# Kernel tuning notes

Hardware: AMD Instinct MI355X
Metric: run time of the kernel (lower is better)

## Reference

```python
import jax, jax.numpy as jnp
import numpy as np
from jax import lax

E = 5      # NUM_EXPERTS
K = 3      # top-k
DIN = 32 * 10 * 10  # 3200
DH = 128
NCLS = 10


def setup_inputs() -> dict:
    key = jax.random.key(0)
    ks = jax.random.split(key, 16)
    s = 0.02
    return {
        "x": jax.random.normal(ks[0], (8192, 1, 28, 28), dtype=jnp.float32),
        "conv1_w": jax.random.normal(ks[1], (16, 1, 5, 5), dtype=jnp.float32) * s,
        "conv1_b": jnp.zeros((16,), jnp.float32),
        "conv2_w": jax.random.normal(ks[2], (32, 16, 3, 3), dtype=jnp.float32) * s,
        "conv2_b": jnp.zeros((32,), jnp.float32),
        "Wg": jax.random.normal(ks[3], (DIN, E), dtype=jnp.float32) * s,
        "bg": jnp.zeros((E,), jnp.float32),
        "Wglu": jax.random.normal(ks[4], (DIN, E), dtype=jnp.float32) * s,
        "bglu": jnp.zeros((E,), jnp.float32),
        "W1e": jax.random.normal(ks[5], (E, DIN, DH), dtype=jnp.float32) * s,
        "b1e": jnp.zeros((E, DH), jnp.float32),
        "W2e": jax.random.normal(ks[6], (E, DH, DH), dtype=jnp.float32) * s,
        "b2e": jnp.zeros((E, DH), jnp.float32),
        "Ws": jax.random.normal(ks[7], (DH, NCLS), dtype=jnp.float32) * s,
        "bs": jnp.zeros((NCLS,), jnp.float32),
    }


def _conv(x, w, b):
    y = lax.conv_general_dilated(x, w, (1, 1), 'VALID',
                                 dimension_numbers=('NCHW', 'OIHW', 'NCHW'))
    return y + b[None, :, None, None]


def _maxpool2(x):
    return lax.reduce_window(x, -jnp.inf, lax.max, (1, 1, 2, 2), (1, 1, 2, 2), 'VALID')


def reference(x, conv1_w, conv1_b, conv2_w, conv2_b, Wg, bg, Wglu, bglu,
              W1e, b1e, W2e, b2e, Ws, bs):
    # conv feature extractor: [B,1,28,28] -> [B,3200]
    h = jax.nn.relu(_conv(x, conv1_w, conv1_b))          # [B,16,24,24]
    h = _maxpool2(h)                                     # [B,16,12,12]
    h = jax.nn.relu(_conv(h, conv2_w, conv2_b))          # [B,32,10,10]
    feat = h.reshape(h.shape[0], -1)                     # [B,3200]

    # GLU-gated router: logits * sigmoid(glu)
    h_act = feat @ Wg + bg                               # [B,E]
    h_glu_act = jax.nn.sigmoid(feat @ Wglu + bglu)       # [B,E]
    gate_logits = h_act * h_glu_act                      # [B,E]

    # top-K routing with softmax over selected logits
    top_v, top_i = lax.top_k(gate_logits, K)             # [B,K]
    top_w = jax.nn.softmax(top_v, axis=-1)               # [B,K]
    onehot = jax.nn.one_hot(top_i, E, dtype=feat.dtype)  # [B,K,E]
    weights = jnp.einsum('bk,bke->be', top_w, onehot)    # [B,E]

    # experts (dense compute of all E=5 experts, masked combine)
    e1 = jnp.tanh(jnp.einsum('bd,edh->beh', feat, W1e) + b1e[None])  # [B,E,128]
    e2 = jnp.tanh(jnp.einsum('beh,ehg->beg', e1, W2e) + b2e[None])   # [B,E,128]
    moe_out = jnp.einsum('beg,be->bg', e2, weights)      # [B,128]

    logits = moe_out @ Ws + bs                           # [B,10]
    return jax.nn.softmax(logits, axis=1)
```

## Files before the change

### kernel.cpp

```cpp
#include <hip/hip_runtime.h>
#include <stdint.h>

typedef unsigned short u16;
typedef __attribute__((ext_vector_type(8))) short bf16x8;
typedef __attribute__((ext_vector_type(4))) float f32x4;

#define MFMA16(a, b, c) __builtin_amdgcn_mfma_f32_16x16x32_bf16((a), (b), (c), 0, 0, 0)
#define GLD16(gp, lp) __builtin_amdgcn_global_load_lds( \
    (__attribute__((address_space(1))) void*)(gp), \
    (__attribute__((address_space(3))) void*)(lp), 16, 0, 0)

__device__ __forceinline__ u16 f2b(float f) {
  uint32_t u = __float_as_uint(f);
  u += 0x7FFFu + ((u >> 16) & 1u);
  return (u16)(u >> 16);
}
__device__ __forceinline__ float tanhfast(float x) {
  float e = __expf(2.f * x);
  return (e - 1.f) / (e + 1.f);
}


__global__ __launch_bounds__(256) void prep_misc_kernel(
    const float* __restrict__ c2w, const float* __restrict__ Wg,
    const float* __restrict__ Wglu, const float* __restrict__ W2e,
    u16* __restrict__ W2colF, u16* __restrict__ WcatT, u16* __restrict__ W2T) {
  int i = blockIdx.x * 256 + threadIdx.x;
  if (i < 5120) {
    int j = i & 7, l = (i >> 3) & 63, nt = (i >> 9) & 1, s = i >> 10;
    int k = s * 32 + ((l >> 4) & 3) * 8 + j;
    int n = (l & 15) + nt * 16;
    float v = 0.f;
    if (k < 144) {
      int kykx = k >> 4, ci = k & 15;
      int ky = kykx / 3, kx = kykx - ky * 3;
      v = c2w[((n * 16 + ci) * 3 + ky) * 3 + kx];
    }
    W2colF[i] = f2b(v);
  } else if (i < 56320) {
    int o = i - 5120;
    int s = o >> 9, rest = o & 511;
    int l = rest >> 3, j = rest & 7;
    int r = l & 15, c = (l >> 4) * 8 + j;
    int dref = c * 100 + s;
    float v = 0.f;
    if (r < 5) v = Wg[dref * 5 + r];
    else if (r < 10) v = Wglu[dref * 5 + (r - 5)];
    WcatT[o] = f2b(v);
  } else if (i < 138240) {
    int o = i - 56320;
    int e = o >> 14, rem = o & 16383;
    int g = rem >> 7, h = rem & 127;
    W2T[o] = f2b(W2e[(e * 128 + h) * 128 + g]);
  }
}

__global__ __launch_bounds__(256) void prep_w1t_kernel(
    const float* __restrict__ W1e, u16* __restrict__ W1T) {
  __shared__ u16 ts[64][128];
  int t = threadIdx.x;
  int e = blockIdx.x / 50, pt = blockIdx.x % 50;
  {
    int r64 = t >> 2;
    int ph = r64 >> 5, c = r64 & 31;
    int d = c * 100 + pt * 2 + ph;
    const float* src = W1e + ((size_t)e * 3200 + d) * 128 + (t & 3) * 32;
    u16* drow = &ts[r64][(t & 3) * 32];
#pragma unroll
    for (int u = 0; u < 8; u++) {
      float4 v = *(const float4*)(src + u * 4);
      drow[u * 4 + 0] = f2b(v.x); drow[u * 4 + 1] = f2b(v.y);
      drow[u * 4 + 2] = f2b(v.z); drow[u * 4 + 3] = f2b(v.w);
    }
  }
  __syncthreads();
#pragma unroll
  for (int k = 0; k < 4; k++) {
    int u = t + k * 256;
    int ph = u >> 9, nb = (u >> 6) & 7, l = u & 63;
    int lm = l & 15, lqf = l >> 4;
    u16 tmp[8];
#pragma unroll
    for (int j = 0; j < 8; j++)
      tmp[j] = ts[ph * 32 + lqf * 8 + j][nb * 16 + lm];
    *(uint4*)(W1T + (((size_t)((e * 100 + pt * 2 + ph) * 8 + nb)) << 9) + l * 8) =
        *(const uint4*)tmp;
  }
}

__global__ __launch_bounds__(256) void conv1_kernel(
    const float* __restrict__ x, const float* __restrict__ w1,
    const float* __restrict__ b1, u16* __restrict__ h1) {
  __shared__ __align__(16) u16 cp[7232];
  int t = threadIdx.x, b = blockIdx.x, w = t >> 6, l = t & 63;

  if (t < 84) {
    int r = (t * 171) >> 9;
    int o = t - r * 3;
    const float4* src = (const float4*)(x + (size_t)b * 784 + r * 28 + o * 8);
    float4 qa = src[0], qb = src[1], qc = src[2];
    float4 qd = {0.f, 0.f, 0.f, 0.f};
    if (o < 2) qd = src[3];
    uint32_t d0 = (uint32_t)f2b(qa.x) | ((uint32_t)f2b(qa.y) << 16);
    uint32_t d1 = (uint32_t)f2b(qa.z) | ((uint32_t)f2b(qa.w) << 16);
    uint32_t d2 = (uint32_t)f2b(qb.x) | ((uint32_t)f2b(qb.y) << 16);
    uint32_t d3 = (uint32_t)f2b(qb.z) | ((uint32_t)f2b(qb.w) << 16);
    uint32_t d4 = (uint32_t)f2b(qc.x) | ((uint32_t)f2b(qc.y) << 16);
    uint32_t d5 = (uint32_t)f2b(qc.z) | ((uint32_t)f2b(qc.w) << 16);
    uint32_t d6 = (uint32_t)f2b(qd.x) | ((uint32_t)f2b(qd.y) << 16);
    uint32_t d7 = (uint32_t)f2b(qd.z) | ((uint32_t)f2b(qd.w) << 16);
#define SH(hi, lo) (((lo) >> 16) | ((hi) << 16))
    int base = r * 32 + o * 8;
    *(uint4*)&cp[base + 0 * 904] = uint4{d0, d1, d2, d3};
    *(uint4*)&cp[base + 1 * 904] = uint4{SH(d1, d0), SH(d2, d1), SH(d3, d2), SH(d4, d3)};
    *(uint4*)&cp[base + 2 * 904] = uint4{d1, d2, d3, d4};
    *(uint4*)&cp[base + 3 * 904] = uint4{SH(d2, d1), SH(d3, d2), SH(d4, d3), SH(d5, d4)};
    *(uint4*)&cp[base + 4 * 904] = uint4{d2, d3, d4, d5};
    *(uint4*)&cp[base + 5 * 904] = uint4{SH(d3, d2), SH(d4, d3), SH(d5, d4), SH(d6, d5)};
    *(uint4*)&cp[base + 6 * 904] = uint4{d3, d4, d5, d6};
    *(uint4*)&cp[base + 7 * 904] = uint4{SH(d4, d3), SH(d5, d4), SH(d6, d5), SH(d7, d6)};
#undef SH
  }

  int lm = l & 15, c = l & 7, ry = (l >> 3) & 1, q = l >> 4;
  bf16x8 bw1 = {0, 0, 0, 0, 0, 0, 0, 0}, bw2 = {0, 0, 0, 0, 0, 0, 0, 0};
#pragma unroll
  for (int j = 0; j < 5; j++) {
    bw1[j] = (short)f2b(w1[lm * 25 + q * 5 + j]);
    if (q == 0) bw2[j] = (short)f2b(w1[lm * 25 + 20 + j]);
  }
  float bias = b1[lm];
  u16* hout = h1 + (size_t)b * 2304;
  __syncthreads();

#pragma unroll
  for (int i = 0; i < 9; i++) {
    int tt = i * 4 + w;
    int p = (tt * 171) >> 9;
    int xo = tt - p * 3;
    int r1 = p * 2 + ry + q;
    int r2 = min(r1 + 4, 27);
    bf16x8 a1 = *(const bf16x8*)&cp[c * 904 + r1 * 32 + xo * 8];
    bf16x8 a2 = *(const bf16x8*)&cp[c * 904 + r2 * 32 + xo * 8];
    f32x4 acc = {0.f, 0.f, 0.f, 0.f};
    acc = MFMA16(a1, bw1, acc);
    acc = MFMA16(a2, bw2, acc);
    float xm0 = fmaxf(acc[0], acc[1]);
    float xm1 = fmaxf(acc[2], acc[3]);
    float ym0 = fmaxf(xm0, __shfl_xor(xm0, 32));
    float ym1 = fmaxf(xm1, __shfl_xor(xm1, 32));
    if (l < 32) {
      int po = (p * 12 + xo * 4 + 2 * q) * 16 + lm;
      hout[po]      = f2b(fmaxf(ym0 + bias, 0.f));
      hout[po + 16] = f2b(fmaxf(ym1 + bias, 0.f));
    }
  }
}

__global__ __launch_bounds__(256) void conv2_kernel(
    const u16* __restrict__ h1, const u16* __restrict__ W2colF,
    const float* __restrict__ b2, u16* __restrict__ feat) {
  __shared__ u16 ct[4][16][32];
  int t = threadIdx.x;
  int w = t >> 6, l = t & 63;
  bf16x8 bfr[5][2];
#pragma unroll
  for (int s = 0; s < 5; s++)
#pragma unroll
    for (int nt = 0; nt < 2; nt++)
      bfr[s][nt] = *(const bf16x8*)(W2colF + ((size_t)(s * 2 + nt) * 64 + l) * 8);
  int lm = l & 15, lq = l >> 4, hi = l >> 5;
  int cib = (lq & 1) * 8;
  float bias0 = b2[lm], bias1 = b2[lm + 16];
  int g0 = blockIdx.x * 128 + w * 32;
#pragma unroll
  for (int sub = 0; sub < 2; sub++) {
    int g = g0 + sub * 16 + lm;
    uint32_t bimg = (uint32_t)(((uint64_t)(uint32_t)g * 1374389535ull) >> 37);
    int p = g - (int)bimg * 100;
    int y = (p * 205) >> 11;
    int xc = p - y * 10;
    const u16* base = h1 + (size_t)bimg * 2304;
    f32x4 acc0 = {0.f, 0.f, 0.f, 0.f}, acc1 = {0.f, 0.f, 0.f, 0.f};
#pragma unroll
    for (int s = 0; s < 5; s++) {
      int kk = 2 * s + hi;
      if (kk > 8) kk = 8;
      int ky = (kk * 11) >> 5;
      int kx = kk - ky * 3;
      int off = ((y + ky) * 12 + (xc + kx)) * 16 + cib;
      bf16x8 a = *(const bf16x8*)(base + off);
      acc0 = MFMA16(a, bfr[s][0], acc0);
      acc1 = MFMA16(a, bfr[s][1], acc1);
    }
#pragma unroll
    for (int rr = 0; rr < 4; rr++) {
      ct[w][lq * 4 + rr][lm]      = f2b(fmaxf(acc0[rr] + bias0, 0.f));
      ct[w][lq * 4 + rr][lm + 16] = f2b(fmaxf(acc1[rr] + bias1, 0.f));
    }
    int gg = g0 + sub * 16 + (l >> 2);
    uint32_t bi2 = (uint32_t)(((uint64_t)(uint32_t)gg * 1374389535ull) >> 37);
    int pp = gg - (int)bi2 * 100;
    int mt2 = (int)(bi2 >> 6), rb = (int)((bi2 >> 4) & 3), lmr = (int)(bi2 & 15);
    uint4 v = *(const uint4*)&ct[w][l >> 2][(l & 3) * 8];
    *(uint4*)(feat + (((size_t)(mt2 * 100 + pp) * 4 + rb) << 9) +
              ((l & 3) * 16 + lmr) * 8) = v;
  }
}

#define GEMM1_KLOOP(HASW, VMCSTR)                                              \
  {                                                                            \
    GLD16(pA, &lds[0][w * 512]);                                               \
    GLD16(pB1, &lds[0][2048 + w * 512]);                                       \
    GLD16(pB2, &lds[0][4096 + w * 512]);                                       \
    if (HASW) GLD16(pW, &lds[0][6144]);                                        \
    pA += 2048; pB1 += 4096; pB2 += 4096; pW += 512;                           \
    for (int s = 0; s < 100; s++) {                                            \
      int buf = s & 1;                                                         \
      if (s < 99) {                                                            \
        GLD16(pA, &lds[buf ^ 1][w * 512]);                                     \
        GLD16(pB1, &lds[buf ^ 1][2048 + w * 512]);                             \
        GLD16(pB2, &lds[buf ^ 1][4096 + w * 512]);                             \
        if (HASW) GLD16(pW, &lds[buf ^ 1][6144]);                              \
        pA += 2048; pB1 += 4096; pB2 += 4096; pW += 512;                       \
        asm volatile("s_waitcnt " VMCSTR ::: "memory");                        \
      } else {                                                                 \
        asm volatile("s_waitcnt vmcnt(0)" ::: "memory");                       \
      }                                                                        \
      asm volatile("s_barrier" ::: "memory");                                  \
      const u16* st = &lds[buf][0];                                            \
      bf16x8 af[2], bf[4];                                                     \
      _Pragma("unroll")                                                        \
      for (int i = 0; i < 2; i++)                                              \
        af[i] = *(const bf16x8*)(st + ((w & 1) * 2 + i) * 512 + l * 8);        \
      _Pragma("unroll")                                                        \
      for (int j = 0; j < 4; j++)                                              \
        bf[j] = *(const bf16x8*)(st + 2048 + ((w >> 1) * 4 + j) * 512 + l * 8);\
      _Pragma("unroll")                                                        \
      for (int i = 0; i < 2; i++)                                              \
        _Pragma("unroll")                                                      \
        for (int j = 0; j < 4; j++)                                            \
          acc[i][j] = MFMA16(af[i], bf[j], acc[i][j]);                         \
      if (HASW && w < 2) {                                                     \
        bf16x8 wf = *(const bf16x8*)(st + 6144 + l * 8);                       \
        racc[0] = MFMA16(af[0], wf, racc[0]);                                  \
        racc[1] = MFMA16(af[1], wf, racc[1]);                                  \
      }                                                                        \
      asm volatile("s_barrier" ::: "memory");                                  \
    }                                                                          \
  }

__global__ __launch_bounds__(256, 3) void gemm1_kernel(
    const u16* __restrict__ feat, const u16* __restrict__ W1T,
    const u16* __restrict__ WcatT, const float* __restrict__ b1e,
    const float* __restrict__ bg, const float* __restrict__ bglu,
    u16* __restrict__ e1b, float* __restrict__ rw) {
  __shared__ u16 lds[2][6656];
  int t = threadIdx.x, w = t >> 6, l = t & 63;
  int mt = blockIdx.x & 127;
  int e = blockIdx.x >> 7;
  size_t m0 = (size_t)mt * 64;
  int lm = l & 15, lq = l >> 4;
  int m_off = (w & 1) * 32, n_off = (w >> 1) * 64;

  const u16* pA = feat + (size_t)mt * 204800 + w * 512 + l * 8;
  const u16* pB1 = W1T + (size_t)e * 409600 + w * 512 + l * 8;
  const u16* pB2 = pB1 + 2048;
  const u16* pW = WcatT + l * 8;

  f32x4 acc[2][4] = {};
  f32x4 racc[2] = {};

  if (e == 0) GEMM1_KLOOP(true, "vmcnt(4)")
  else        GEMM1_KLOOP(false, "vmcnt(3)")

  float b1v[4];
#pragma unroll
  for (int j = 0; j < 4; j++) b1v[j] = b1e[e * 128 + n_off + 16 * j + lm];
  u16* E1t = &lds[0][0];
#pragma unroll
  for (int i = 0; i < 2; i++)
#pragma unroll
    for (int j = 0; j < 4; j++)
#pragma unroll
      for (int rr = 0; rr < 4; rr++) {
        int row = m_off + 16 * i + lq * 4 + rr;
        int col = n_off + 16 * j + lm;
        E1t[row * 128 + col] = f2b(tanhfast(acc[i][j][rr] + b1v[j]));
      }
  if (e == 0 && w < 2) {
    float* RACC = (float*)((char*)lds + 20480);
#pragma unroll
    for (int i = 0; i < 2; i++)
#pragma unroll
      for (int rr = 0; rr < 4; rr++)
        RACC[(m_off + 16 * i + lq * 4 + rr) * 16 + lm] = racc[i][rr];
  }
  __syncthreads();
#pragma unroll
  for (int k2 = 0; k2 < 4; k2++) {
    int u = t + k2 * 256;
    int row = u >> 4, sc = u & 15;
    uint4 v = *(const uint4*)(E1t + row * 128 + sc * 8);
    *(uint4*)(e1b + (m0 + row) * 640 + e * 128 + sc * 8) = v;
  }
  if (e == 0 && t < 64) {
    const float* RACC = (const float*)((char*)lds + 20480);
    float gt[5];
#pragma unroll
    for (int ee = 0; ee < 5; ee++) {
      float va = RACC[t * 16 + ee] + bg[ee];
      float vb = RACC[t * 16 + 5 + ee] + bglu[ee];
      gt[ee] = va * (1.f / (1.f + __expf(-vb)));
    }
    float w3[3]; int i3[3];
    unsigned used = 0;
#pragma unroll
    for (int k = 0; k < 3; k++) {
      float best = -1e30f; int bi = 0;
#pragma unroll
      for (int ee = 0; ee < 5; ee++)
        if (!((used >> ee) & 1u) && gt[ee] > best) { best = gt[ee]; bi = ee; }
      used |= 1u << bi; w3[k] = best; i3[k] = bi;
    }
    float s1 = __expf(w3[1] - w3[0]), s2 = __expf(w3[2] - w3[0]);
    float inv = 1.f / (1.f + s1 + s2);
    float o[5] = {0.f, 0.f, 0.f, 0.f, 0.f};
    o[i3[0]] = inv; o[i3[1]] = s1 * inv; o[i3[2]] = s2 * inv;
#pragma unroll
    for (int ee = 0; ee < 5; ee++) rw[(m0 + t) * 5 + ee] = o[ee];
  }
}

__global__ __launch_bounds__(256) void gemm2_head_kernel(
    const u16* __restrict__ e1b, const u16* __restrict__ W2T,
    const float* __restrict__ b2e, const float* __restrict__ rw,
    const float* __restrict__ Ws, const float* __restrict__ bs,
    float* __restrict__ out) {
  __shared__ u16 E1s[32][648];
  __shared__ float wssh[1280];
  __shared__ float rws[160];
  int t = threadIdx.x;
  int r0 = blockIdx.x * 32;
  {
    int row = t >> 3;
    const u16* src = e1b + (size_t)(r0 + row) * 640 + (t & 7) * 8;
    u16* drow = &E1s[row][(t & 7) * 8];
#pragma unroll
    for (int k = 0; k < 10; k++)
      *(uint4*)(drow + k * 64) = *(const uint4*)(src + k * 64);
  }
  if (t < 160) rws[t] = rw[r0 * 5 + t];
  for (int i = t; i < 1280; i += 256) wssh[i] = Ws[i];
  __syncthreads();

  int w = t >> 6, l = t & 63, lm = l & 15, lq = l >> 4;
  int mh = w & 1, nh = w >> 1;
  f32x4 moeacc[4] = {};
#pragma unroll
  for (int e = 0; e < 5; e++) {
    f32x4 acc[4] = {};
    const u16* w2e = W2T + e * 16384;
#pragma unroll
    for (int kk = 0; kk < 4; kk++) {
      bf16x8 a = *(const bf16x8*)&E1s[mh * 16 + lm][e * 128 + kk * 32 + lq * 8];
#pragma unroll
      for (int j = 0; j < 4; j++) {
        bf16x8 b = *(const bf16x8*)(w2e + (nh * 64 + 16 * j + lm) * 128 + kk * 32 + lq * 8);
        acc[j] = MFMA16(a, b, acc[j]);
      }
    }
#pragma unroll
    for (int j = 0; j < 4; j++) {
      float b2v = b2e[e * 128 + nh * 64 + 16 * j + lm];
#pragma unroll
      for (int rr = 0; rr < 4; rr++) {
        float v = tanhfast(acc[j][rr] + b2v);
        moeacc[j][rr] += rws[(mh * 16 + lq * 4 + rr) * 5 + e] * v;
      }
    }
  }
  __syncthreads();
  float* moes = (float*)&E1s[0][0];
#pragma unroll
  for (int j = 0; j < 4; j++)
#pragma unroll
    for (int rr = 0; rr < 4; rr++)
      moes[(mh * 16 + lq * 4 + rr) * 132 + nh * 64 + 16 * j + lm] = moeacc[j][rr];
  __syncthreads();
  float* parts = moes + 32 * 132;
  if (t < 128) {
    int row = t >> 2, qc = t & 3;
    float pl[10] = {};
    for (int cc = qc * 32; cc < qc * 32 + 32; cc++) {
      float mv = moes[row * 132 + cc];
#pragma unroll
      for (int cls = 0; cls < 10; cls++) pl[cls] += mv * wssh[cc * 10 + cls];
    }
#pragma unroll
    for (int cls = 0; cls < 10; cls++) parts[(row * 4 + qc) * 10 + cls] = pl[cls];
  }
  __syncthreads();
  if (t < 32) {
    float lg[10];
    float mx = -1e30f;
#pragma unroll
    for (int cls = 0; cls < 10; cls++) {
      lg[cls] = parts[(t * 4) * 10 + cls] + parts[(t * 4 + 1) * 10 + cls] +
                parts[(t * 4 + 2) * 10 + cls] + parts[(t * 4 + 3) * 10 + cls] + bs[cls];
      mx = fmaxf(mx, lg[cls]);
    }
    float sum = 0.f;
#pragma unroll
    for (int cls = 0; cls < 10; cls++) { lg[cls] = __expf(lg[cls] - mx); sum += lg[cls]; }
    float inv = 1.f / sum;
    float* orow = out + (size_t)(r0 + t) * 10;
#pragma unroll
    for (int cls = 0; cls < 10; cls++) orow[cls] = lg[cls] * inv;
  }
}

extern "C" void kernel_launch(void* const* d_in, const int* in_sizes, int n_in,
                              void* d_out, int out_size, void* d_ws, size_t ws_size,
                              hipStream_t stream) {
  const float* x    = (const float*)d_in[0];
  const float* c1w  = (const float*)d_in[1];
  const float* c1b  = (const float*)d_in[2];
  const float* c2w  = (const float*)d_in[3];
  const float* c2b  = (const float*)d_in[4];
  const float* Wg   = (const float*)d_in[5];
  const float* bg   = (const float*)d_in[6];
  const float* Wglu = (const float*)d_in[7];
  const float* bglu = (const float*)d_in[8];
  const float* W1e  = (const float*)d_in[9];
  const float* b1e  = (const float*)d_in[10];
  const float* W2e  = (const float*)d_in[11];
  const float* b2e  = (const float*)d_in[12];
  const float* Wsp  = (const float*)d_in[13];
  const float* bsp  = (const float*)d_in[14];
  char* ws = (char*)d_ws;
  u16* h1      = (u16*)(ws + 0);
  u16* e1b     = (u16*)(ws + 0);
  u16* feat    = (u16*)(ws + 37748736);
  u16* W1T     = (u16*)(ws + 90177536);
  u16* W2T     = (u16*)(ws + 94273536);
  u16* W2colF  = (u16*)(ws + 94437376);
  u16* WcatT   = (u16*)(ws + 94447616);
  float* rw    = (float*)(ws + 94550016);

  prep_misc_kernel<<<540, 256, 0, stream>>>(c2w, Wg, Wglu, W2e, W2colF, WcatT, W2T);
  prep_w1t_kernel<<<250, 256, 0, stream>>>(W1e, W1T);
  conv1_kernel<<<8192, 256, 0, stream>>>(x, c1w, c1b, h1);
  conv2_kernel<<<6400, 256, 0, stream>>>(h1, W2colF, c2b, feat);
  gemm1_kernel<<<640, 256, 0, stream>>>(feat, W1T, WcatT, b1e, bg, bglu, e1b, rw);
  gemm2_head_kernel<<<256, 256, 0, stream>>>(e1b, W2T, b2e, rw, Wsp, bsp,
                                             (float*)d_out);
}
```

Before: 230.0 us.

## Load GEMM1 fragments directly from global memory, dropping LDS double buffering

Replaces the LDS-staged, double-buffered K loop in gemm1 (global_load_lds plus barriers) with direct per-wave global loads of pre-swizzled bf16 fragments into registers. The loop is unrolled by two, and launch bounds rise to four blocks per CU because LDS is now needed only for the epilogue. The aim is to remove barrier and LDS traffic and raise occupancy. In exchange, each fragment is fetched from global memory by two waves instead of once, and there is no explicit prefetch, so latency hiding depends on occupancy and the compiler's scheduling.

```diff
diff --git a/kernel.cpp b/kernel.cpp
--- a/kernel.cpp
+++ b/kernel.cpp
@@ -6,9 +6,6 @@
 typedef __attribute__((ext_vector_type(4))) float f32x4;
 
 #define MFMA16(a, b, c) __builtin_amdgcn_mfma_f32_16x16x32_bf16((a), (b), (c), 0, 0, 0)
-#define GLD16(gp, lp) __builtin_amdgcn_global_load_lds( \
-    (__attribute__((address_space(1))) void*)(gp), \
-    (__attribute__((address_space(3))) void*)(lp), 16, 0, 0)
 
 __device__ __forceinline__ u16 f2b(float f) {
   uint32_t u = __float_as_uint(f);
@@ -208,76 +205,55 @@
   }
 }
 
-#define GEMM1_KLOOP(HASW, VMCSTR)                                              \
-  {                                                                            \
-    GLD16(pA, &lds[0][w * 512]);                                               \
-    GLD16(pB1, &lds[0][2048 + w * 512]);                                       \
-    GLD16(pB2, &lds[0][4096 + w * 512]);                                       \
-    if (HASW) GLD16(pW, &lds[0][6144]);                                        \
-    pA += 2048; pB1 += 4096; pB2 += 4096; pW += 512;                           \
-    for (int s = 0; s < 100; s++) {                                            \
-      int buf = s & 1;                                                         \
-      if (s < 99) {                                                            \
-        GLD16(pA, &lds[buf ^ 1][w * 512]);                                     \
-        GLD16(pB1, &lds[buf ^ 1][2048 + w * 512]);                             \
-        GLD16(pB2, &lds[buf ^ 1][4096 + w * 512]);                             \
-        if (HASW) GLD16(pW, &lds[buf ^ 1][6144]);                              \
-        pA += 2048; pB1 += 4096; pB2 += 4096; pW += 512;                       \
-        asm volatile("s_waitcnt " VMCSTR ::: "memory");                        \
-      } else {                                                                 \
-        asm volatile("s_waitcnt vmcnt(0)" ::: "memory");                       \
-      }                                                                        \
-      asm volatile("s_barrier" ::: "memory");                                  \
-      const u16* st = &lds[buf][0];                                            \
-      bf16x8 af[2], bf[4];                                                     \
-      _Pragma("unroll")                                                        \
-      for (int i = 0; i < 2; i++)                                              \
-        af[i] = *(const bf16x8*)(st + ((w & 1) * 2 + i) * 512 + l * 8);        \
-      _Pragma("unroll")                                                        \
-      for (int j = 0; j < 4; j++)                                              \
-        bf[j] = *(const bf16x8*)(st + 2048 + ((w >> 1) * 4 + j) * 512 + l * 8);\
-      _Pragma("unroll")                                                        \
-      for (int i = 0; i < 2; i++)                                              \
-        _Pragma("unroll")                                                      \
-        for (int j = 0; j < 4; j++)                                            \
-          acc[i][j] = MFMA16(af[i], bf[j], acc[i][j]);                         \
-      if (HASW && w < 2) {                                                     \
-        bf16x8 wf = *(const bf16x8*)(st + 6144 + l * 8);                       \
-        racc[0] = MFMA16(af[0], wf, racc[0]);                                  \
-        racc[1] = MFMA16(af[1], wf, racc[1]);                                  \
-      }                                                                        \
-      asm volatile("s_barrier" ::: "memory");                                  \
-    }                                                                          \
-  }
-
-__global__ __launch_bounds__(256, 3) void gemm1_kernel(
+__global__ __launch_bounds__(256, 4) void gemm1_kernel(
     const u16* __restrict__ feat, const u16* __restrict__ W1T,
     const u16* __restrict__ WcatT, const float* __restrict__ b1e,
     const float* __restrict__ bg, const float* __restrict__ bglu,
     u16* __restrict__ e1b, float* __restrict__ rw) {
-  __shared__ u16 lds[2][6656];
+  __shared__ u16 E1t[8192];
+  __shared__ float RACC[1024];
   int t = threadIdx.x, w = t >> 6, l = t & 63;
   int mt = blockIdx.x & 127;
   int e = blockIdx.x >> 7;
   size_t m0 = (size_t)mt * 64;
   int lm = l & 15, lq = l >> 4;
   int m_off = (w & 1) * 32, n_off = (w >> 1) * 64;
-
-  const u16* pA = feat + (size_t)mt * 204800 + w * 512 + l * 8;
-  const u16* pB1 = W1T + (size_t)e * 409600 + w * 512 + l * 8;
-  const u16* pB2 = pB1 + 2048;
+  bool rwave = (e == 0) && (w < 2);
+
+  const u16* pA = feat + (size_t)mt * 204800 + ((w & 1) * 2) * 512 + l * 8;
+  const u16* pB = W1T + (size_t)e * 409600 + ((w >> 1) * 4) * 512 + l * 8;
   const u16* pW = WcatT + l * 8;
 
   f32x4 acc[2][4] = {};
   f32x4 racc[2] = {};
 
-  if (e == 0) GEMM1_KLOOP(true, "vmcnt(4)")
-  else        GEMM1_KLOOP(false, "vmcnt(3)")
+#pragma unroll 2
+  for (int s = 0; s < 100; s++) {
+    bf16x8 af0 = *(const bf16x8*)(pA);
+    bf16x8 af1 = *(const bf16x8*)(pA + 512);
+    bf16x8 bf0 = *(const bf16x8*)(pB);
+    bf16x8 bf1 = *(const bf16x8*)(pB + 512);
+    bf16x8 bf2 = *(const bf16x8*)(pB + 1024);
+    bf16x8 bf3 = *(const bf16x8*)(pB + 1536);
+    acc[0][0] = MFMA16(af0, bf0, acc[0][0]);
+    acc[0][1] = MFMA16(af0, bf1, acc[0][1]);
+    acc[0][2] = MFMA16(af0, bf2, acc[0][2]);
+    acc[0][3] = MFMA16(af0, bf3, acc[0][3]);
+    acc[1][0] = MFMA16(af1, bf0, acc[1][0]);
+    acc[1][1] = MFMA16(af1, bf1, acc[1][1]);
+    acc[1][2] = MFMA16(af1, bf2, acc[1][2]);
+    acc[1][3] = MFMA16(af1, bf3, acc[1][3]);
+    if (rwave) {
+      bf16x8 wf = *(const bf16x8*)(pW);
+      racc[0] = MFMA16(af0, wf, racc[0]);
+      racc[1] = MFMA16(af1, wf, racc[1]);
+    }
+    pA += 2048; pB += 4096; pW += 512;
+  }
 
   float b1v[4];
 #pragma unroll
   for (int j = 0; j < 4; j++) b1v[j] = b1e[e * 128 + n_off + 16 * j + lm];
-  u16* E1t = &lds[0][0];
 #pragma unroll
   for (int i = 0; i < 2; i++)
 #pragma unroll
@@ -288,8 +264,7 @@
         int col = n_off + 16 * j + lm;
         E1t[row * 128 + col] = f2b(tanhfast(acc[i][j][rr] + b1v[j]));
       }
-  if (e == 0 && w < 2) {
-    float* RACC = (float*)((char*)lds + 20480);
+  if (rwave) {
 #pragma unroll
     for (int i = 0; i < 2; i++)
 #pragma unroll
@@ -305,7 +280,6 @@
     *(uint4*)(e1b + (m0 + row) * 640 + e * 128 + sc * 8) = v;
   }
   if (e == 0 && t < 64) {
-    const float* RACC = (const float*)((char*)lds + 20480);
     float gt[5];
 #pragma unroll
     for (int ee = 0; ee < 5; ee++) {
```

New measurement: 270.3 us. 1.18x slower.

## Fuse conv1 and conv2 into one per-image kernel using LDS

Applied to the files above, without the earlier changes.

Merges the conv1 and conv2 kernels so each block computes one image's pooled conv1 output into shared memory and then runs the conv2 MFMA tiles directly from it. This removes the global write and reread of the intermediate h1 tensor and one kernel launch. In exchange, conv2 work is split per image into 7 tiles over 4 waves, which leaves some waves idle and wastes a padded tile. LDS use per block also rises, which may reduce occupancy.

```diff
diff --git a/kernel.cpp b/kernel.cpp
--- a/kernel.cpp
+++ b/kernel.cpp
@@ -88,10 +88,12 @@
   }
 }
 
-__global__ __launch_bounds__(256) void conv1_kernel(
+__global__ __launch_bounds__(256) void conv_fused_kernel(
     const float* __restrict__ x, const float* __restrict__ w1,
-    const float* __restrict__ b1, u16* __restrict__ h1) {
+    const float* __restrict__ b1, const u16* __restrict__ W2colF,
+    const float* __restrict__ b2, u16* __restrict__ feat) {
   __shared__ __align__(16) u16 cp[7232];
+  __shared__ __align__(16) u16 h1s[2304];
   int t = threadIdx.x, b = blockIdx.x, w = t >> 6, l = t & 63;
 
   if (t < 84) {
@@ -130,7 +132,6 @@
     if (q == 0) bw2[j] = (short)f2b(w1[lm * 25 + 20 + j]);
   }
   float bias = b1[lm];
-  u16* hout = h1 + (size_t)b * 2304;
   __syncthreads();
 
 #pragma unroll
@@ -151,36 +152,29 @@
     float ym1 = fmaxf(xm1, __shfl_xor(xm1, 32));
     if (l < 32) {
       int po = (p * 12 + xo * 4 + 2 * q) * 16 + lm;
-      hout[po]      = f2b(fmaxf(ym0 + bias, 0.f));
-      hout[po + 16] = f2b(fmaxf(ym1 + bias, 0.f));
-    }
-  }
-}
-
-__global__ __launch_bounds__(256) void conv2_kernel(
-    const u16* __restrict__ h1, const u16* __restrict__ W2colF,
-    const float* __restrict__ b2, u16* __restrict__ feat) {
-  __shared__ u16 ct[4][16][32];
-  int t = threadIdx.x;
-  int w = t >> 6, l = t & 63;
+      h1s[po]      = f2b(fmaxf(ym0 + bias, 0.f));
+      h1s[po + 16] = f2b(fmaxf(ym1 + bias, 0.f));
+    }
+  }
+
   bf16x8 bfr[5][2];
 #pragma unroll
   for (int s = 0; s < 5; s++)
 #pragma unroll
     for (int nt = 0; nt < 2; nt++)
       bfr[s][nt] = *(const bf16x8*)(W2colF + ((size_t)(s * 2 + nt) * 64 + l) * 8);
-  int lm = l & 15, lq = l >> 4, hi = l >> 5;
+  int lq = l >> 4, hi = l >> 5;
   int cib = (lq & 1) * 8;
   float bias0 = b2[lm], bias1 = b2[lm + 16];
-  int g0 = blockIdx.x * 128 + w * 32;
-#pragma unroll
-  for (int sub = 0; sub < 2; sub++) {
-    int g = g0 + sub * 16 + lm;
-    uint32_t bimg = (uint32_t)(((uint64_t)(uint32_t)g * 1374389535ull) >> 37);
-    int p = g - (int)bimg * 100;
-    int y = (p * 205) >> 11;
-    int xc = p - y * 10;
-    const u16* base = h1 + (size_t)bimg * 2304;
+  int mt2 = b >> 6, rb = (b >> 4) & 3, lmr = b & 15;
+  u16* ct = cp;
+  __syncthreads();
+
+  for (int ti = w; ti < 7; ti += 4) {
+    int p = ti * 16 + lm;
+    int pc = p < 100 ? p : 99;
+    int y = (pc * 205) >> 11;
+    int xc = pc - y * 10;
     f32x4 acc0 = {0.f, 0.f, 0.f, 0.f}, acc1 = {0.f, 0.f, 0.f, 0.f};
 #pragma unroll
     for (int s = 0; s < 5; s++) {
@@ -189,22 +183,21 @@
       int ky = (kk * 11) >> 5;
       int kx = kk - ky * 3;
       int off = ((y + ky) * 12 + (xc + kx)) * 16 + cib;
-      bf16x8 a = *(const bf16x8*)(base + off);
+      bf16x8 a = *(const bf16x8*)&h1s[off];
       acc0 = MFMA16(a, bfr[s][0], acc0);
       acc1 = MFMA16(a, bfr[s][1], acc1);
     }
 #pragma unroll
     for (int rr = 0; rr < 4; rr++) {
-      ct[w][lq * 4 + rr][lm]      = f2b(fmaxf(acc0[rr] + bias0, 0.f));
-      ct[w][lq * 4 + rr][lm + 16] = f2b(fmaxf(acc1[rr] + bias1, 0.f));
-    }
-    int gg = g0 + sub * 16 + (l >> 2);
-    uint32_t bi2 = (uint32_t)(((uint64_t)(uint32_t)gg * 1374389535ull) >> 37);
-    int pp = gg - (int)bi2 * 100;
-    int mt2 = (int)(bi2 >> 6), rb = (int)((bi2 >> 4) & 3), lmr = (int)(bi2 & 15);
-    uint4 v = *(const uint4*)&ct[w][l >> 2][(l & 3) * 8];
-    *(uint4*)(feat + (((size_t)(mt2 * 100 + pp) * 4 + rb) << 9) +
-              ((l & 3) * 16 + lmr) * 8) = v;
+      ct[w * 512 + (lq * 4 + rr) * 32 + lm]      = f2b(fmaxf(acc0[rr] + bias0, 0.f));
+      ct[w * 512 + (lq * 4 + rr) * 32 + lm + 16] = f2b(fmaxf(acc1[rr] + bias1, 0.f));
+    }
+    int pp = ti * 16 + (l >> 2);
+    if (pp < 100) {
+      uint4 v = *(const uint4*)&ct[w * 512 + (l >> 2) * 32 + (l & 3) * 8];
+      *(uint4*)(feat + (((size_t)(mt2 * 100 + pp) * 4 + rb) << 9) +
+                ((l & 3) * 16 + lmr) * 8) = v;
+    }
   }
 }
 
@@ -439,7 +432,6 @@
   const float* Wsp  = (const float*)d_in[13];
   const float* bsp  = (const float*)d_in[14];
   char* ws = (char*)d_ws;
-  u16* h1      = (u16*)(ws + 0);
   u16* e1b     = (u16*)(ws + 0);
   u16* feat    = (u16*)(ws + 37748736);
   u16* W1T     = (u16*)(ws + 90177536);
@@ -450,8 +442,7 @@
 
   prep_misc_kernel<<<540, 256, 0, stream>>>(c2w, Wg, Wglu, W2e, W2colF, WcatT, W2T);
   prep_w1t_kernel<<<250, 256, 0, stream>>>(W1e, W1T);
-  conv1_kernel<<<8192, 256, 0, stream>>>(x, c1w, c1b, h1);
-  conv2_kernel<<<6400, 256, 0, stream>>>(h1, W2colF, c2b, feat);
+  conv_fused_kernel<<<8192, 256, 0, stream>>>(x, c1w, c1b, W2colF, c2b, feat);
   gemm1_kernel<<<640, 256, 0, stream>>>(feat, W1T, WcatT, b1e, bg, bglu, e1b, rw);
   gemm2_head_kernel<<<256, 256, 0, stream>>>(e1b, W2T, b2e, rw, Wsp, bsp,
                                              (float*)d_out);
```

New measurement: 211.3 us. -8.1%, faster.
